# Optimization experiments

Measured on AMD Instinct MI355X. Metric: run time of the kernel, lower is better.

Reference implementation:

```python
import jax, jax.numpy as jnp
import numpy as np

B, S, D = 2, 1024, 2048
L = 4
HQ, HKV, HD = 32, 8, 64
I = 5632
V = 32000
EPS = 1e-5
THETA = 10000.0
SCALE = HD ** -0.5
GROUP = HQ // HKV


def setup_inputs() -> dict:
    key = jax.random.key(0)
    ks = jax.random.split(key, 8)
    s = 0.02
    return {
        "input_ids": jax.random.randint(ks[0], (B, S), 0, V, dtype=jnp.int32),
        "positions": jnp.broadcast_to(jnp.arange(S, dtype=jnp.int32), (B, S)),
        "embed": jax.random.normal(ks[1], (V, D), jnp.float32) * s,
        "w_qkv": jax.random.normal(ks[2], (L, D, (HQ + 2 * HKV) * HD), jnp.float32) * s,
        "w_o": jax.random.normal(ks[3], (L, HQ * HD, D), jnp.float32) * s,
        "w_gate_up": jax.random.normal(ks[4], (L, D, 2 * I), jnp.float32) * s,
        "w_down": jax.random.normal(ks[5], (L, I, D), jnp.float32) * s,
        "ln1_w": jnp.ones((L, D), jnp.float32),
        "ln2_w": jnp.ones((L, D), jnp.float32),
        "norm_w": jnp.ones((D,), jnp.float32),
    }


def rmsnorm(x, w):
    var = jnp.mean(x * x, axis=-1, keepdims=True)
    return x * jax.lax.rsqrt(var + EPS) * w


def rope(positions, x):
    # x: [B, S, H, HD]; neox-style rotate-half RoPE
    inv_freq = 1.0 / (THETA ** (jnp.arange(0, HD, 2, dtype=jnp.float32) / HD))
    ang = positions.astype(jnp.float32)[..., None] * inv_freq  # [B, S, HD/2]
    cos = jnp.cos(ang)[:, :, None, :]
    sin = jnp.sin(ang)[:, :, None, :]
    x1, x2 = jnp.split(x, 2, axis=-1)
    return jnp.concatenate([x1 * cos - x2 * sin, x2 * cos + x1 * sin], axis=-1)


def llama_forward(input_ids, positions, embed, w_qkv, w_o, w_gate_up, w_down,
                  ln1_w, ln2_w, norm_w):
    h = embed[input_ids]                      # [B, S, D]
    res = jnp.zeros_like(h)
    causal = jnp.tril(jnp.ones((S, S), dtype=bool))
    neg = jnp.asarray(jnp.finfo(h.dtype).min, h.dtype)

    def layer(carry, params):
        h, res = carry
        wqkv, wo, wgu, wd, l1, l2 = params
        # fused RMSNorm + residual-add (vllm RMSNorm(x, residual) semantics)
        res = h + res
        h = rmsnorm(res, l1)
        # QKV projection + RoPE
        qkv = h @ wqkv
        q, k, v = jnp.split(qkv, [HQ * HD, (HQ + HKV) * HD], axis=-1)
        q = q.reshape(B, S, HQ, HD)
        k = k.reshape(B, S, HKV, HD)
        v = v.reshape(B, S, HKV, HD)
        q = rope(positions, q)
        k = rope(positions, k)
        # GQA: broadcast kv heads across query groups
        k = jnp.repeat(k, GROUP, axis=2)      # [B, S, HQ, HD]
        v = jnp.repeat(v, GROUP, axis=2)
        scores = jnp.einsum('bqhd,bkhd->bhqk', q, k) * SCALE
        scores = jnp.where(causal, scores, neg)
        attn = jax.nn.softmax(scores, axis=-1)
        o = jnp.einsum('bhqk,bkhd->bqhd', attn, v).reshape(B, S, HQ * HD)
        h = o @ wo
        # post-attention fused RMSNorm + residual
        res = h + res
        h = rmsnorm(res, l2)
        # SwiGLU MLP
        gu = h @ wgu
        g, u = jnp.split(gu, 2, axis=-1)
        h = (jax.nn.silu(g) * u) @ wd
        return (h, res), None

    (h, res), _ = jax.lax.scan(layer, (h, res),
                               (w_qkv, w_o, w_gate_up, w_down, ln1_w, ln2_w))
    return rmsnorm(h + res, norm_w)


def reference(input_ids, positions, embed, w_qkv, w_o, w_gate_up, w_down,
              ln1_w, ln2_w, norm_w):
    return llama_forward(input_ids, positions, embed, w_qkv, w_o, w_gate_up,
                         w_down, ln1_w, ln2_w, norm_w)
```

## Files before the change

### kernel.cpp

```cpp
#include <hip/hip_runtime.h>
#include <hip/hip_bf16.h>

#define B_ 2
#define S_ 1024
#define T_ (B_*S_)
#define D_ 2048
#define L_ 4
#define HQ_ 32
#define HKV_ 8
#define HD_ 64
#define I_ 5632
#define EPS_ 1e-5f
#define SCALE_ 0.125f

typedef __attribute__((ext_vector_type(4))) float  float4v;
typedef __attribute__((ext_vector_type(8))) short  short8v;

#define GLOAD16(g, l) \
  __builtin_amdgcn_global_load_lds((const __attribute__((address_space(1))) void*)(g), \
                                   (__attribute__((address_space(3))) void*)(l), 16, 0, 0)

__device__ __forceinline__ short f2bf(float f) {
  union { float f; unsigned u; } c; c.f = f;
  unsigned u = c.u + 0x7fffu + ((c.u >> 16) & 1u);
  return (short)(u >> 16);
}

__device__ __forceinline__ void xcd_swizzle(int gx, int gy, int& bx, int& by) {
  int nwg = gx * gy;
  int orig = by * gx + bx;
  int q = nwg >> 3, r = nwg & 7;
  int xcd = orig & 7, loc = orig >> 3;
  int swz = (xcd < r ? xcd * (q + 1) : r * (q + 1) + (xcd - r) * q) + loc;
  bx = swz / gy;
  by = swz - bx * gy;
}

__global__ __launch_bounds__(256)
void transpose_bf16(const float* __restrict__ in, short* __restrict__ out,
                    int K, int N) {
  __shared__ float t[64][65];
  const int bx = blockIdx.x * 64;
  const int by = blockIdx.y * 64;
  const int tid = threadIdx.x;
  const int lr = tid >> 4;
  const int lc = (tid & 15) * 4;
  #pragma unroll
  for (int j = 0; j < 64; j += 16) {
    float4v v = *(const float4v*)(in + (size_t)(by + lr + j) * N + bx + lc);
    t[lr + j][lc] = v[0]; t[lr + j][lc + 1] = v[1];
    t[lr + j][lc + 2] = v[2]; t[lr + j][lc + 3] = v[3];
  }
  __syncthreads();
  const int nr = tid >> 3;
  const int kc = (tid & 7) * 8;
  #pragma unroll
  for (int j = 0; j < 64; j += 32) {
    short8v y;
    #pragma unroll
    for (int e = 0; e < 8; e++) y[e] = f2bf(t[kc + e][nr + j]);
    *(short8v*)(out + (size_t)(bx + nr + j) * K + by + kc) = y;
  }
}

__global__ __launch_bounds__(256)
void embed_gather(const int* __restrict__ ids, const float* __restrict__ embed,
                  float* __restrict__ h) {
  size_t i = (size_t)blockIdx.x * 256 + threadIdx.x;
  int t  = (int)(i >> 9);
  int d4 = (int)(i & 511);
  ((float4v*)h)[i] = ((const float4v*)(embed + (size_t)ids[t] * D_))[d4];
}

__global__ __launch_bounds__(256)
void rmsnorm_kernel(const float* __restrict__ x, float* __restrict__ res,
                    const float* __restrict__ w, void* __restrict__ outp,
                    int first, int bf16out) {
  const int row = blockIdx.x;
  const int tid = threadIdx.x;
  const size_t base = (size_t)row * D_;
  float4v v0, v1;
  if (first) {
    v0 = ((const float4v*)(x + base))[tid * 2];
    v1 = ((const float4v*)(x + base))[tid * 2 + 1];
    ((float4v*)(res + base))[tid * 2]     = v0;
    ((float4v*)(res + base))[tid * 2 + 1] = v1;
  } else {
    v0 = ((const float4v*)(res + base))[tid * 2];
    v1 = ((const float4v*)(res + base))[tid * 2 + 1];
  }
  float ss = v0[0]*v0[0] + v0[1]*v0[1] + v0[2]*v0[2] + v0[3]*v0[3]
           + v1[0]*v1[0] + v1[1]*v1[1] + v1[2]*v1[2] + v1[3]*v1[3];
  #pragma unroll
  for (int off = 32; off > 0; off >>= 1) ss += __shfl_xor(ss, off, 64);
  __shared__ float red[4];
  if ((tid & 63) == 0) red[tid >> 6] = ss;
  __syncthreads();
  float tot = red[0] + red[1] + red[2] + red[3];
  float rs = rsqrtf(tot * (1.0f / D_) + EPS_);
  float4v w0 = ((const float4v*)w)[tid * 2];
  float4v w1 = ((const float4v*)w)[tid * 2 + 1];
  float4v o0 = v0 * rs * w0;
  float4v o1 = v1 * rs * w1;
  if (bf16out) {
    short8v y;
    #pragma unroll
    for (int k = 0; k < 4; k++) { y[k] = f2bf(o0[k]); y[k + 4] = f2bf(o1[k]); }
    ((short8v*)((char*)outp + base * 2))[tid] = y;
  } else {
    float* op = (float*)outp + base;
    ((float4v*)op)[tid * 2]     = o0;
    ((float4v*)op)[tid * 2 + 1] = o1;
  }
}

__global__ __launch_bounds__(512, 4)
void gemm_big128(const short* __restrict__ A, const short* __restrict__ Bt,
                 float* __restrict__ C, int M, int N, int K, int addto) {
  __shared__ short sA[2][128 * 64];
  __shared__ short sB[2][128 * 64];
  int bx = blockIdx.x, by = blockIdx.y;
  xcd_swizzle(gridDim.x, gridDim.y, bx, by);
  const int tid  = threadIdx.x;
  const int lane = tid & 63;
  const int wv   = tid >> 6;
  const int wr   = wv >> 2;
  const int wc   = wv & 3;
  const int row0 = by * 128;
  const int col0 = bx * 128;
  const int fr = lane & 15;
  const int g  = lane >> 4;
  const int NT = K >> 6;

  float4v acc[4][2] = {};

  int rS[2], cS[2];
  #pragma unroll
  for (int k = 0; k < 2; k++) {
    int s = tid + k * 512;
    rS[k] = s >> 3;
    cS[k] = (((s & 7) ^ (rS[k] & 7)) << 3);
  }

#define STAGE128(t, buf) do { \
    int k0_ = (t) << 6; \
    _Pragma("unroll") \
    for (int k_ = 0; k_ < 2; k_++) \
      GLOAD16(A  + (size_t)(row0 + rS[k_]) * K + k0_ + cS[k_], \
              &sA[buf][(tid + k_ * 512) * 8]); \
    _Pragma("unroll") \
    for (int k_ = 0; k_ < 2; k_++) \
      GLOAD16(Bt + (size_t)(col0 + rS[k_]) * K + k0_ + cS[k_], \
              &sB[buf][(tid + k_ * 512) * 8]); \
  } while (0)

  STAGE128(0, 0);

  for (int t = 0; t < NT; t++) {
    const int cur = t & 1;
    if (t + 1 < NT) {
      STAGE128(t + 1, cur ^ 1);
      asm volatile("s_waitcnt vmcnt(4)" ::: "memory");
    } else {
      asm volatile("s_waitcnt vmcnt(0)" ::: "memory");
    }
    __builtin_amdgcn_s_barrier();
    __builtin_amdgcn_sched_barrier(0);

    const short* pA = &sA[cur][(wr * 64) * 64];
    const short* pB = &sB[cur][(wc * 32) * 64];
    #pragma unroll
    for (int ks = 0; ks < 2; ks++) {
      const int fswk = ((((ks << 2) | g) ^ (fr & 7)) << 3);
      short8v bfr[2], afr[4];
      #pragma unroll
      for (int ni = 0; ni < 2; ni++)
        bfr[ni] = *(const short8v*)(pB + (ni * 16 + fr) * 64 + fswk);
      #pragma unroll
      for (int m4 = 0; m4 < 4; m4++)
        afr[m4] = *(const short8v*)(pA + (m4 * 16 + fr) * 64 + fswk);
      __builtin_amdgcn_s_setprio(1);
      #pragma unroll
      for (int m4 = 0; m4 < 4; m4++)
        #pragma unroll
        for (int ni = 0; ni < 2; ni++)
          acc[m4][ni] = __builtin_amdgcn_mfma_f32_16x16x32_bf16(
              afr[m4], bfr[ni], acc[m4][ni], 0, 0, 0);
      __builtin_amdgcn_s_setprio(0);
    }
    asm volatile("" ::: "memory");
    __builtin_amdgcn_s_barrier();
  }

  #pragma unroll
  for (int m4 = 0; m4 < 4; m4++)
    #pragma unroll
    for (int ni = 0; ni < 2; ni++) {
      size_t base = (size_t)(row0 + wr * 64 + m4 * 16 + g * 4) * N
                    + col0 + wc * 32 + ni * 16 + fr;
      if (addto) {
        #pragma unroll
        for (int r = 0; r < 4; r++)
          C[base + (size_t)r * N] += acc[m4][ni][r];
      } else {
        #pragma unroll
        for (int r = 0; r < 4; r++)
          C[base + (size_t)r * N] = acc[m4][ni][r];
      }
    }
#undef STAGE128
}

__global__ __launch_bounds__(512, 2)
void gemm_glu_big(const short* __restrict__ A, const short* __restrict__ Bt,
                  short* __restrict__ mlp, int K) {
  __shared__ short sA[2][128 * 64];
  __shared__ short sG[2][128 * 64];
  __shared__ short sU[2][128 * 64];
  int bx = blockIdx.x, by = blockIdx.y;
  xcd_swizzle(gridDim.x, gridDim.y, bx, by);
  const int tid  = threadIdx.x;
  const int lane = tid & 63;
  const int wv   = tid >> 6;
  const int wr   = wv >> 2;
  const int wc   = wv & 3;
  const int row0 = by * 128;
  const int col0 = bx * 128;
  const int fr = lane & 15;
  const int g  = lane >> 4;
  const int NT = K >> 6;

  float4v accg[4][2] = {};
  float4v accu[4][2] = {};

  int rS[2], cS[2];
  #pragma unroll
  for (int k = 0; k < 2; k++) {
    int s = tid + k * 512;
    rS[k] = s >> 3;
    cS[k] = (((s & 7) ^ (rS[k] & 7)) << 3);
  }

#define STAGEGLU(t, buf) do { \
    int k0_ = (t) << 6; \
    _Pragma("unroll") \
    for (int k_ = 0; k_ < 2; k_++) \
      GLOAD16(A  + (size_t)(row0 + rS[k_]) * K + k0_ + cS[k_], \
              &sA[buf][(tid + k_ * 512) * 8]); \
    _Pragma("unroll") \
    for (int k_ = 0; k_ < 2; k_++) \
      GLOAD16(Bt + (size_t)(col0 + rS[k_]) * K + k0_ + cS[k_], \
              &sG[buf][(tid + k_ * 512) * 8]); \
    _Pragma("unroll") \
    for (int k_ = 0; k_ < 2; k_++) \
      GLOAD16(Bt + (size_t)(col0 + I_ + rS[k_]) * K + k0_ + cS[k_], \
              &sU[buf][(tid + k_ * 512) * 8]); \
  } while (0)

  STAGEGLU(0, 0);

  for (int t = 0; t < NT; t++) {
    const int cur = t & 1;
    if (t + 1 < NT) {
      STAGEGLU(t + 1, cur ^ 1);
      asm volatile("s_waitcnt vmcnt(6)" ::: "memory");
    } else {
      asm volatile("s_waitcnt vmcnt(0)" ::: "memory");
    }
    __builtin_amdgcn_s_barrier();
    __builtin_amdgcn_sched_barrier(0);

    const short* pA = &sA[cur][(wr * 64) * 64];
    const short* pG = &sG[cur][(wc * 32) * 64];
    const short* pU = &sU[cur][(wc * 32) * 64];
    #pragma unroll
    for (int ks = 0; ks < 2; ks++) {
      const int fswk = ((((ks << 2) | g) ^ (fr & 7)) << 3);
      short8v bg[2], bu[2], afr[4];
      #pragma unroll
      for (int ni = 0; ni < 2; ni++) {
        bg[ni] = *(const short8v*)(pG + (ni * 16 + fr) * 64 + fswk);
        bu[ni] = *(const short8v*)(pU + (ni * 16 + fr) * 64 + fswk);
      }
      #pragma unroll
      for (int m4 = 0; m4 < 4; m4++)
        afr[m4] = *(const short8v*)(pA + (m4 * 16 + fr) * 64 + fswk);
      __builtin_amdgcn_s_setprio(1);
      #pragma unroll
      for (int m4 = 0; m4 < 4; m4++)
        #pragma unroll
        for (int ni = 0; ni < 2; ni++) {
          accg[m4][ni] = __builtin_amdgcn_mfma_f32_16x16x32_bf16(
              afr[m4], bg[ni], accg[m4][ni], 0, 0, 0);
          accu[m4][ni] = __builtin_amdgcn_mfma_f32_16x16x32_bf16(
              afr[m4], bu[ni], accu[m4][ni], 0, 0, 0);
        }
      __builtin_amdgcn_s_setprio(0);
    }
    asm volatile("" ::: "memory");
    __builtin_amdgcn_s_barrier();
  }

  #pragma unroll
  for (int m4 = 0; m4 < 4; m4++)
    #pragma unroll
    for (int ni = 0; ni < 2; ni++) {
      size_t base = (size_t)(row0 + wr * 64 + m4 * 16 + g * 4) * I_
                    + col0 + wc * 32 + ni * 16 + fr;
      #pragma unroll
      for (int r = 0; r < 4; r++) {
        float gv = accg[m4][ni][r], uv = accu[m4][ni][r];
        mlp[base + (size_t)r * I_] = f2bf(gv / (1.0f + __expf(-gv)) * uv);
      }
    }
#undef STAGEGLU
}

__global__ __launch_bounds__(512, 4)
void gemm_qkv_big(const short* __restrict__ A, const short* __restrict__ Bt,
                  const float* __restrict__ tab, short* __restrict__ qbf,
                  short* __restrict__ kbf, short* __restrict__ vbf, int K) {
  __shared__ short sA[2][128 * 64];
  __shared__ short sB[2][128 * 64];
  int bx = blockIdx.x, by = blockIdx.y;
  xcd_swizzle(gridDim.x, gridDim.y, bx, by);
  const int tid  = threadIdx.x;
  const int lane = tid & 63;
  const int wv   = tid >> 6;
  const int wm   = (wv >> 1) * 32;
  const int wn   = (wv & 1) * 64;
  const int row0 = by * 128;
  const int col0 = bx * 128;
  const int fr = lane & 15;
  const int g  = lane >> 4;
  const int NT = K >> 6;

  float4v acc[2][4] = {};

  int rS[2], cS[2];
  #pragma unroll
  for (int k = 0; k < 2; k++) {
    int s = tid + k * 512;
    rS[k] = s >> 3;
    cS[k] = (((s & 7) ^ (rS[k] & 7)) << 3);
  }

#define STAGEQKV(t, buf) do { \
    int k0_ = (t) << 6; \
    _Pragma("unroll") \
    for (int k_ = 0; k_ < 2; k_++) \
      GLOAD16(A  + (size_t)(row0 + rS[k_]) * K + k0_ + cS[k_], \
              &sA[buf][(tid + k_ * 512) * 8]); \
    _Pragma("unroll") \
    for (int k_ = 0; k_ < 2; k_++) \
      GLOAD16(Bt + (size_t)(col0 + rS[k_]) * K + k0_ + cS[k_], \
              &sB[buf][(tid + k_ * 512) * 8]); \
  } while (0)

  STAGEQKV(0, 0);

  for (int t = 0; t < NT; t++) {
    const int cur = t & 1;
    if (t + 1 < NT) {
      STAGEQKV(t + 1, cur ^ 1);
      asm volatile("s_waitcnt vmcnt(4)" ::: "memory");
    } else {
      asm volatile("s_waitcnt vmcnt(0)" ::: "memory");
    }
    __builtin_amdgcn_s_barrier();
    __builtin_amdgcn_sched_barrier(0);

    const short* pA = &sA[cur][wm * 64];
    const short* pB = &sB[cur][wn * 64];
    #pragma unroll
    for (int ks = 0; ks < 2; ks++) {
      const int fswk = ((((ks << 2) | g) ^ (fr & 7)) << 3);
      short8v afr[2], bfr[4];
      #pragma unroll
      for (int m2 = 0; m2 < 2; m2++)
        afr[m2] = *(const short8v*)(pA + (m2 * 16 + fr) * 64 + fswk);
      #pragma unroll
      for (int ni = 0; ni < 4; ni++)
        bfr[ni] = *(const short8v*)(pB + (ni * 16 + fr) * 64 + fswk);
      __builtin_amdgcn_s_setprio(1);
      #pragma unroll
      for (int m2 = 0; m2 < 2; m2++)
        #pragma unroll
        for (int ni = 0; ni < 4; ni++)
          acc[m2][ni] = __builtin_amdgcn_mfma_f32_16x16x32_bf16(
              afr[m2], bfr[ni], acc[m2][ni], 0, 0, 0);
      __builtin_amdgcn_s_setprio(0);
    }
    asm volatile("" ::: "memory");
    __builtin_amdgcn_s_barrier();
  }

  const int head = (col0 + wn) >> 6;
  if (head < HQ_ + HKV_) {
    const float sc = (head < HQ_) ? SCALE_ : 1.0f;
    short* dst = (head < HQ_) ? qbf : kbf;
    const int hh = (head < HQ_) ? head : head - HQ_;
    const int HN = (head < HQ_) ? HQ_ : HKV_;
    #pragma unroll
    for (int m2 = 0; m2 < 2; m2++)
      #pragma unroll
      for (int jj = 0; jj < 2; jj++)
        #pragma unroll
        for (int r = 0; r < 4; r++) {
          int m = row0 + wm + m2 * 16 + g * 4 + r;
          int b = m >> 10, s = m & (S_ - 1);
          int d1 = jj * 16 + fr;
          float x1 = acc[m2][jj][r], x2 = acc[m2][jj + 2][r];
          const float* tb = tab + (size_t)m * 64 + d1 * 2;
          float c = tb[0], sn = tb[1];
          size_t base = ((size_t)((b * HN + hh) * S_ + s)) * HD_;
          dst[base + d1]      = f2bf((x1 * c - x2 * sn) * sc);
          dst[base + d1 + 32] = f2bf((x2 * c + x1 * sn) * sc);
        }
  } else {
    const int vh = head - HQ_ - HKV_;
    #pragma unroll
    for (int m2 = 0; m2 < 2; m2++)
      #pragma unroll
      for (int ni = 0; ni < 4; ni++)
        #pragma unroll
        for (int r = 0; r < 4; r++) {
          int m = row0 + wm + m2 * 16 + g * 4 + r;
          int b = m >> 10, s = m & (S_ - 1);
          vbf[((size_t)((b * HKV_ + vh) * S_ + s)) * HD_ + ni * 16 + fr] =
              f2bf(acc[m2][ni][r]);
        }
  }
#undef STAGEQKV
}

__global__ __launch_bounds__(256)
void rope_table(const int* __restrict__ pos, float* __restrict__ tab) {
  int i = blockIdx.x * 256 + threadIdx.x;
  int t = i >> 5, ii = i & 31;
  float p = (float)pos[t];
  float freq = __expf(-(float)ii * (9.210340371976184f / 32.0f));
  float ang = p * freq;
  tab[2 * i]     = cosf(ang);
  tab[2 * i + 1] = sinf(ang);
}

#define KPAD 68

__global__ __launch_bounds__(256)
void transpose_v(const short* __restrict__ vbf, short* __restrict__ vtbf) {
  __shared__ short sv[64 * KPAD];
  const int jt = blockIdx.x, kh = blockIdx.y, b = blockIdx.z;
  const int tid = threadIdx.x;
  const short* src = vbf + ((size_t)((b * HKV_ + kh) * S_ + jt * 64)) * HD_;
  #pragma unroll
  for (int it = 0; it < 2; it++) {
    int c = it * 256 + tid;
    int rr = c >> 3, ch = (c & 7) * 8;
    *(short8v*)(&sv[rr * KPAD + ch]) = *(const short8v*)(src + (size_t)rr * HD_ + ch);
  }
  __syncthreads();
  const int dc = tid >> 2;
  const int jc = (tid & 3) * 16;
  short8v o1, o2;
  #pragma unroll
  for (int k = 0; k < 8; k++) o1[k] = sv[(jc + k) * KPAD + dc];
  #pragma unroll
  for (int k = 0; k < 8; k++) o2[k] = sv[(jc + 8 + k) * KPAD + dc];
  short* od = vtbf + ((size_t)((b * HKV_ + kh) * HD_ + dc)) * S_ + jt * 64 + jc;
  *(short8v*)od       = o1;
  *(short8v*)(od + 8) = o2;
}

__global__ __launch_bounds__(256)
void attn_mfma(const short* __restrict__ qbf, const short* __restrict__ kbf,
               const short* __restrict__ vtbf, short* __restrict__ obf) {
  __shared__ short sK[64 * KPAD];
  __shared__ short sVt[64 * KPAD];
  __shared__ short sP[4][16 * KPAD];
  const int qb = blockIdx.x;
  const int h  = blockIdx.y;
  const int b  = blockIdx.z;
  const int kh = h >> 2;
  const int tid  = threadIdx.x;
  const int lane = tid & 63;
  const int wv   = tid >> 6;
  const int q0 = qb * 64;
  const int cc = lane & 15;
  const int g  = lane >> 4;

  short8v qf0, qf1;
  {
    const short* qrow = qbf + ((size_t)((b * HQ_ + h) * S_ + q0 + wv * 16 + cc)) * HD_;
    qf0 = *(const short8v*)(qrow + g * 8);
    qf1 = *(const short8v*)(qrow + g * 8 + 32);
  }
  float4v accO[4] = {};
  float m_r[4], l_r[4];
  #pragma unroll
  for (int r = 0; r < 4; r++) { m_r[r] = -1e30f; l_r[r] = 0.f; }

  const short* kb = kbf  + ((size_t)(b * HKV_ + kh)) * S_ * HD_;
  const short* vb = vtbf + ((size_t)(b * HKV_ + kh)) * HD_ * S_;

  const int rr0 = tid >> 3;
  const int ch0 = (tid & 7) * 8;
  const int rr1 = 32 + rr0;

  short8v kr0 = *(const short8v*)(kb + (size_t)rr0 * HD_ + ch0);
  short8v kr1 = *(const short8v*)(kb + (size_t)rr1 * HD_ + ch0);
  short8v vr0 = *(const short8v*)(vb + (size_t)rr0 * S_ + ch0);
  short8v vr1 = *(const short8v*)(vb + (size_t)rr1 * S_ + ch0);

  for (int jt = 0; jt <= qb; jt++) {
    const int j0 = jt * 64;
    __syncthreads();
    *(short8v*)(&sK[rr0 * KPAD + ch0])  = kr0;
    *(short8v*)(&sK[rr1 * KPAD + ch0])  = kr1;
    *(short8v*)(&sVt[rr0 * KPAD + ch0]) = vr0;
    *(short8v*)(&sVt[rr1 * KPAD + ch0]) = vr1;
    __syncthreads();

    if (jt < qb) {
      const int j0n = j0 + 64;
      kr0 = *(const short8v*)(kb + (size_t)(j0n + rr0) * HD_ + ch0);
      kr1 = *(const short8v*)(kb + (size_t)(j0n + rr1) * HD_ + ch0);
      vr0 = *(const short8v*)(vb + (size_t)rr0 * S_ + j0n + ch0);
      vr1 = *(const short8v*)(vb + (size_t)rr1 * S_ + j0n + ch0);
    }

    float4v sc[4] = {};
    #pragma unroll
    for (int ct = 0; ct < 4; ct++) {
      short8v k0 = *(const short8v*)(&sK[(ct * 16 + cc) * KPAD + g * 8]);
      short8v k1 = *(const short8v*)(&sK[(ct * 16 + cc) * KPAD + g * 8 + 32]);
      __builtin_amdgcn_s_setprio(1);
      sc[ct] = __builtin_amdgcn_mfma_f32_16x16x32_bf16(qf0, k0, sc[ct], 0, 0, 0);
      sc[ct] = __builtin_amdgcn_mfma_f32_16x16x32_bf16(qf1, k1, sc[ct], 0, 0, 0);
      __builtin_amdgcn_s_setprio(0);
    }
    if (jt == qb) {
      #pragma unroll
      for (int ct = 0; ct < 4; ct++)
        #pragma unroll
        for (int r = 0; r < 4; r++)
          if (j0 + ct * 16 + cc > q0 + wv * 16 + g * 4 + r) sc[ct][r] = -1e30f;
    }
    float pmv[4], dmax = -1e30f;
    #pragma unroll
    for (int r = 0; r < 4; r++) {
      float pm = fmaxf(fmaxf(sc[0][r], sc[1][r]), fmaxf(sc[2][r], sc[3][r]));
      pm = fmaxf(pm, __shfl_xor(pm, 1, 64));
      pm = fmaxf(pm, __shfl_xor(pm, 2, 64));
      pm = fmaxf(pm, __shfl_xor(pm, 4, 64));
      pm = fmaxf(pm, __shfl_xor(pm, 8, 64));
      pmv[r] = pm;
      dmax = fmaxf(dmax, pm - m_r[r]);
    }
    if (!__all(dmax <= 8.0f)) {
      float corr[4];
      #pragma unroll
      for (int r = 0; r < 4; r++) {
        float mn = fmaxf(m_r[r], pmv[r]);
        corr[r] = __expf(m_r[r] - mn);
        m_r[r] = mn;
        l_r[r] *= corr[r];
      }
      #pragma unroll
      for (int dt = 0; dt < 4; dt++)
        #pragma unroll
        for (int r = 0; r < 4; r++)
          accO[dt][r] *= corr[r];
    }
    #pragma unroll
    for (int r = 0; r < 4; r++) {
      float rs = 0.f;
      #pragma unroll
      for (int ct = 0; ct < 4; ct++) {
        float p = __expf(sc[ct][r] - m_r[r]);
        sc[ct][r] = p;
        rs += p;
      }
      rs += __shfl_xor(rs, 1, 64);
      rs += __shfl_xor(rs, 2, 64);
      rs += __shfl_xor(rs, 4, 64);
      rs += __shfl_xor(rs, 8, 64);
      l_r[r] += rs;
    }
    #pragma unroll
    for (int ct = 0; ct < 4; ct++)
      #pragma unroll
      for (int r = 0; r < 4; r++)
        sP[wv][(g * 4 + r) * KPAD + ct * 16 + cc] = f2bf(sc[ct][r]);
    short8v pf0 = *(const short8v*)(&sP[wv][cc * KPAD + g * 8]);
    short8v pf1 = *(const short8v*)(&sP[wv][cc * KPAD + g * 8 + 32]);
    #pragma unroll
    for (int dt = 0; dt < 4; dt++) {
      short8v v0 = *(const short8v*)(&sVt[(dt * 16 + cc) * KPAD + g * 8]);
      short8v v1 = *(const short8v*)(&sVt[(dt * 16 + cc) * KPAD + g * 8 + 32]);
      __builtin_amdgcn_s_setprio(1);
      accO[dt] = __builtin_amdgcn_mfma_f32_16x16x32_bf16(pf0, v0, accO[dt], 0, 0, 0);
      accO[dt] = __builtin_amdgcn_mfma_f32_16x16x32_bf16(pf1, v1, accO[dt], 0, 0, 0);
      __builtin_amdgcn_s_setprio(0);
    }
  }
  #pragma unroll
  for (int dt = 0; dt < 4; dt++)
    #pragma unroll
    for (int r = 0; r < 4; r++) {
      int q = q0 + wv * 16 + g * 4 + r;
      obf[((size_t)(b * S_ + q)) * 2048 + h * 64 + dt * 16 + cc] = f2bf(accO[dt][r] / l_r[r]);
    }
}

extern "C" void kernel_launch(void* const* d_in, const int* in_sizes, int n_in,
                              void* d_out, int out_size, void* d_ws, size_t ws_size,
                              hipStream_t stream) {
  const int*   ids   = (const int*)d_in[0];
  const int*   pos   = (const int*)d_in[1];
  const float* embed = (const float*)d_in[2];
  const float* w_qkv = (const float*)d_in[3];
  const float* w_o   = (const float*)d_in[4];
  const float* w_gu  = (const float*)d_in[5];
  const float* w_dn  = (const float*)d_in[6];
  const float* ln1   = (const float*)d_in[7];
  const float* ln2   = (const float*)d_in[8];
  const float* normw = (const float*)d_in[9];
  float* out = (float*)d_out;

  char* p = (char*)d_ws;
  short* wT    = (short*)p; p += (size_t)11264 * 2048 * 2;
  float* h     = (float*)p; p += (size_t)T_ * D_ * 4;
  float* res   = (float*)p; p += (size_t)T_ * D_ * 4;
  short* hnbf  = (short*)p; p += (size_t)T_ * D_ * 2;
  short* obf   = (short*)p; p += (size_t)T_ * D_ * 2;
  short* mlpbf = (short*)p; p += (size_t)T_ * I_ * 2;
  float* tab   = (float*)p; p += (size_t)T_ * 64 * 4;
  short* qbf   = (short*)p; p += (size_t)B_ * HQ_ * S_ * HD_ * 2;
  short* kbf   = (short*)p; p += (size_t)B_ * HKV_ * S_ * HD_ * 2;
  short* vbf   = (short*)p; p += (size_t)B_ * HKV_ * S_ * HD_ * 2;
  short* vtbf  = (short*)p; p += (size_t)B_ * HKV_ * HD_ * S_ * 2;

  embed_gather<<<T_ * D_ / 4 / 256, 256, 0, stream>>>(ids, embed, h);
  rope_table<<<T_ * 32 / 256, 256, 0, stream>>>(pos, tab);

  for (int l = 0; l < L_; l++) {
    rmsnorm_kernel<<<T_, 256, 0, stream>>>(h, res, ln1 + l * D_, hnbf,
                                           l == 0 ? 1 : 0, 1);

    transpose_bf16<<<dim3(3072 / 64, 2048 / 64), 256, 0, stream>>>(
        w_qkv + (size_t)l * 2048 * 3072, wT, 2048, 3072);
    gemm_qkv_big<<<dim3(3072 / 128, T_ / 128), 512, 0, stream>>>(
        hnbf, wT, tab, qbf, kbf, vbf, 2048);

    transpose_v<<<dim3(16, 8, 2), 256, 0, stream>>>(vbf, vtbf);
    attn_mfma<<<dim3(16, 32, 2), 256, 0, stream>>>(qbf, kbf, vtbf, obf);

    transpose_bf16<<<dim3(2048 / 64, 2048 / 64), 256, 0, stream>>>(
        w_o + (size_t)l * 2048 * 2048, wT, 2048, 2048);
    gemm_big128<<<dim3(2048 / 128, T_ / 128), 512, 0, stream>>>(
        obf, wT, res, T_, 2048, 2048, 1);

    rmsnorm_kernel<<<T_, 256, 0, stream>>>(nullptr, res, ln2 + l * D_, hnbf, 0, 1);

    transpose_bf16<<<dim3(11264 / 64, 2048 / 64), 256, 0, stream>>>(
        w_gu + (size_t)l * 2048 * 11264, wT, 2048, 11264);
    gemm_glu_big<<<dim3(I_ / 128, T_ / 128), 512, 0, stream>>>(
        hnbf, wT, mlpbf, 2048);

    transpose_bf16<<<dim3(2048 / 64, 5632 / 64), 256, 0, stream>>>(
        w_dn + (size_t)l * 5632 * 2048, wT, 5632, 2048);
    gemm_big128<<<dim3(2048 / 128, T_ / 128), 512, 0, stream>>>(
        mlpbf, wT, res, T_, 2048, 5632, 1);
  }
  rmsnorm_kernel<<<T_, 256, 0, stream>>>(nullptr, res, normw, out, 0, 0);
}
```

Baseline: 1.739 ms.

## Batch weight transposes into one launch, fuse V transpose, widen attention blocks

Transposes and converts to bf16 the weights of all four layers in a single kernel launch, writing them into dedicated per-layer workspace buffers instead of running sixteen separate transposes inside the layer loop. The QKV GEMM epilogue now writes V directly in transposed layout, so the separate transpose_v kernel is removed. Attention blocks grow to 512 threads covering 128 queries each, which halves the block count and shares each K/V tile load across more waves. The cost is a larger workspace and a new causal-mask condition over the last two key tiles of each block.

```diff
diff --git a/kernel.cpp b/kernel.cpp
--- a/kernel.cpp
+++ b/kernel.cpp
@@ -15,6 +15,7 @@
 
 typedef __attribute__((ext_vector_type(4))) float  float4v;
 typedef __attribute__((ext_vector_type(8))) short  short8v;
+typedef __attribute__((ext_vector_type(4))) short  short4v;
 
 #define GLOAD16(g, l) \
   __builtin_amdgcn_global_load_lds((const __attribute__((address_space(1))) void*)(g), \
@@ -37,11 +38,24 @@
 }
 
 __global__ __launch_bounds__(256)
-void transpose_bf16(const float* __restrict__ in, short* __restrict__ out,
-                    int K, int N) {
+void transpose_all(const float* __restrict__ wq, const float* __restrict__ wo,
+                   const float* __restrict__ wg, const float* __restrict__ wd,
+                   short* __restrict__ tq, short* __restrict__ to_,
+                   short* __restrict__ tg, short* __restrict__ td) {
+  const int l = blockIdx.y;
+  int id = blockIdx.x;
+  const float* in; short* out; int K, N, bxt, byt;
+  if (id < 1536)      { in = wq + (size_t)l * 2048 * 3072;  out = tq + (size_t)l * 2048 * 3072;
+                        K = 2048; N = 3072;  bxt = id % 48;  byt = id / 48; }
+  else if (id < 2560) { id -= 1536; in = wo + (size_t)l * 2048 * 2048; out = to_ + (size_t)l * 2048 * 2048;
+                        K = 2048; N = 2048;  bxt = id % 32;  byt = id / 32; }
+  else if (id < 8192) { id -= 2560; in = wg + (size_t)l * 2048 * 11264; out = tg + (size_t)l * 2048 * 11264;
+                        K = 2048; N = 11264; bxt = id % 176; byt = id / 176; }
+  else                { id -= 8192; in = wd + (size_t)l * 5632 * 2048; out = td + (size_t)l * 5632 * 2048;
+                        K = 5632; N = 2048;  bxt = id % 32;  byt = id / 32; }
   __shared__ float t[64][65];
-  const int bx = blockIdx.x * 64;
-  const int by = blockIdx.y * 64;
+  const int bx = bxt * 64;
+  const int by = byt * 64;
   const int tid = threadIdx.x;
   const int lr = tid >> 4;
   const int lc = (tid & 15) * 4;
@@ -319,7 +333,7 @@
 __global__ __launch_bounds__(512, 4)
 void gemm_qkv_big(const short* __restrict__ A, const short* __restrict__ Bt,
                   const float* __restrict__ tab, short* __restrict__ qbf,
-                  short* __restrict__ kbf, short* __restrict__ vbf, int K) {
+                  short* __restrict__ kbf, short* __restrict__ vtbf, int K) {
   __shared__ short sA[2][128 * 64];
   __shared__ short sB[2][128 * 64];
   int bx = blockIdx.x, by = blockIdx.y;
@@ -420,16 +434,18 @@
   } else {
     const int vh = head - HQ_ - HKV_;
     #pragma unroll
-    for (int m2 = 0; m2 < 2; m2++)
-      #pragma unroll
-      for (int ni = 0; ni < 4; ni++)
-        #pragma unroll
-        for (int r = 0; r < 4; r++) {
-          int m = row0 + wm + m2 * 16 + g * 4 + r;
-          int b = m >> 10, s = m & (S_ - 1);
-          vbf[((size_t)((b * HKV_ + vh) * S_ + s)) * HD_ + ni * 16 + fr] =
-              f2bf(acc[m2][ni][r]);
-        }
+    for (int m2 = 0; m2 < 2; m2++) {
+      int m0 = row0 + wm + m2 * 16 + g * 4;
+      int b = m0 >> 10, s0 = m0 & (S_ - 1);
+      #pragma unroll
+      for (int ni = 0; ni < 4; ni++) {
+        int d = ni * 16 + fr;
+        short4v w;
+        #pragma unroll
+        for (int r = 0; r < 4; r++) w[r] = f2bf(acc[m2][ni][r]);
+        *(short4v*)(&vtbf[((size_t)((b * HKV_ + vh) * HD_ + d)) * S_ + s0]) = w;
+      }
+    }
   }
 #undef STAGEQKV
 }
@@ -447,37 +463,12 @@
 
 #define KPAD 68
 
-__global__ __launch_bounds__(256)
-void transpose_v(const short* __restrict__ vbf, short* __restrict__ vtbf) {
-  __shared__ short sv[64 * KPAD];
-  const int jt = blockIdx.x, kh = blockIdx.y, b = blockIdx.z;
-  const int tid = threadIdx.x;
-  const short* src = vbf + ((size_t)((b * HKV_ + kh) * S_ + jt * 64)) * HD_;
-  #pragma unroll
-  for (int it = 0; it < 2; it++) {
-    int c = it * 256 + tid;
-    int rr = c >> 3, ch = (c & 7) * 8;
-    *(short8v*)(&sv[rr * KPAD + ch]) = *(const short8v*)(src + (size_t)rr * HD_ + ch);
-  }
-  __syncthreads();
-  const int dc = tid >> 2;
-  const int jc = (tid & 3) * 16;
-  short8v o1, o2;
-  #pragma unroll
-  for (int k = 0; k < 8; k++) o1[k] = sv[(jc + k) * KPAD + dc];
-  #pragma unroll
-  for (int k = 0; k < 8; k++) o2[k] = sv[(jc + 8 + k) * KPAD + dc];
-  short* od = vtbf + ((size_t)((b * HKV_ + kh) * HD_ + dc)) * S_ + jt * 64 + jc;
-  *(short8v*)od       = o1;
-  *(short8v*)(od + 8) = o2;
-}
-
-__global__ __launch_bounds__(256)
+__global__ __launch_bounds__(512)
 void attn_mfma(const short* __restrict__ qbf, const short* __restrict__ kbf,
                const short* __restrict__ vtbf, short* __restrict__ obf) {
   __shared__ short sK[64 * KPAD];
   __shared__ short sVt[64 * KPAD];
-  __shared__ short sP[4][16 * KPAD];
+  __shared__ short sP[8][16 * KPAD];
   const int qb = blockIdx.x;
   const int h  = blockIdx.y;
   const int b  = blockIdx.z;
@@ -485,7 +476,7 @@
   const int tid  = threadIdx.x;
   const int lane = tid & 63;
   const int wv   = tid >> 6;
-  const int q0 = qb * 64;
+  const int q0 = qb * 128;
   const int cc = lane & 15;
   const int g  = lane >> 4;
 
@@ -503,30 +494,24 @@
   const short* kb = kbf  + ((size_t)(b * HKV_ + kh)) * S_ * HD_;
   const short* vb = vtbf + ((size_t)(b * HKV_ + kh)) * HD_ * S_;
 
-  const int rr0 = tid >> 3;
-  const int ch0 = (tid & 7) * 8;
-  const int rr1 = 32 + rr0;
-
-  short8v kr0 = *(const short8v*)(kb + (size_t)rr0 * HD_ + ch0);
-  short8v kr1 = *(const short8v*)(kb + (size_t)rr1 * HD_ + ch0);
-  short8v vr0 = *(const short8v*)(vb + (size_t)rr0 * S_ + ch0);
-  short8v vr1 = *(const short8v*)(vb + (size_t)rr1 * S_ + ch0);
-
-  for (int jt = 0; jt <= qb; jt++) {
+  const int rr = tid >> 3;
+  const int ch = (tid & 7) * 8;
+
+  short8v kr = *(const short8v*)(kb + (size_t)rr * HD_ + ch);
+  short8v vr = *(const short8v*)(vb + (size_t)rr * S_ + ch);
+
+  const int nb = 2 * qb + 1;
+  for (int jt = 0; jt <= nb; jt++) {
     const int j0 = jt * 64;
     __syncthreads();
-    *(short8v*)(&sK[rr0 * KPAD + ch0])  = kr0;
-    *(short8v*)(&sK[rr1 * KPAD + ch0])  = kr1;
-    *(short8v*)(&sVt[rr0 * KPAD + ch0]) = vr0;
-    *(short8v*)(&sVt[rr1 * KPAD + ch0]) = vr1;
+    *(short8v*)(&sK[rr * KPAD + ch])  = kr;
+    *(short8v*)(&sVt[rr * KPAD + ch]) = vr;
     __syncthreads();
 
-    if (jt < qb) {
+    if (jt < nb) {
       const int j0n = j0 + 64;
-      kr0 = *(const short8v*)(kb + (size_t)(j0n + rr0) * HD_ + ch0);
-      kr1 = *(const short8v*)(kb + (size_t)(j0n + rr1) * HD_ + ch0);
-      vr0 = *(const short8v*)(vb + (size_t)rr0 * S_ + j0n + ch0);
-      vr1 = *(const short8v*)(vb + (size_t)rr1 * S_ + j0n + ch0);
+      kr = *(const short8v*)(kb + (size_t)(j0n + rr) * HD_ + ch);
+      vr = *(const short8v*)(vb + (size_t)rr * S_ + j0n + ch);
     }
 
     float4v sc[4] = {};
@@ -539,7 +524,7 @@
       sc[ct] = __builtin_amdgcn_mfma_f32_16x16x32_bf16(qf1, k1, sc[ct], 0, 0, 0);
       __builtin_amdgcn_s_setprio(0);
     }
-    if (jt == qb) {
+    if (jt >= 2 * qb) {
       #pragma unroll
       for (int ct = 0; ct < 4; ct++)
         #pragma unroll
@@ -629,7 +614,10 @@
   float* out = (float*)d_out;
 
   char* p = (char*)d_ws;
-  short* wT    = (short*)p; p += (size_t)11264 * 2048 * 2;
+  short* wTq  = (short*)p; p += (size_t)L_ * 2048 * 3072 * 2;
+  short* wTo  = (short*)p; p += (size_t)L_ * 2048 * 2048 * 2;
+  short* wTgu = (short*)p; p += (size_t)L_ * 2048 * 11264 * 2;
+  short* wTdn = (short*)p; p += (size_t)L_ * 5632 * 2048 * 2;
   float* h     = (float*)p; p += (size_t)T_ * D_ * 4;
   float* res   = (float*)p; p += (size_t)T_ * D_ * 4;
   short* hnbf  = (short*)p; p += (size_t)T_ * D_ * 2;
@@ -638,9 +626,10 @@
   float* tab   = (float*)p; p += (size_t)T_ * 64 * 4;
   short* qbf   = (short*)p; p += (size_t)B_ * HQ_ * S_ * HD_ * 2;
   short* kbf   = (short*)p; p += (size_t)B_ * HKV_ * S_ * HD_ * 2;
-  short* vbf   = (short*)p; p += (size_t)B_ * HKV_ * S_ * HD_ * 2;
   short* vtbf  = (short*)p; p += (size_t)B_ * HKV_ * HD_ * S_ * 2;
 
+  transpose_all<<<dim3(11008, L_), 256, 0, stream>>>(
+      w_qkv, w_o, w_gu, w_dn, wTq, wTo, wTgu, wTdn);
   embed_gather<<<T_ * D_ / 4 / 256, 256, 0, stream>>>(ids, embed, h);
   rope_table<<<T_ * 32 / 256, 256, 0, stream>>>(pos, tab);
 
@@ -648,30 +637,21 @@
     rmsnorm_kernel<<<T_, 256, 0, stream>>>(h, res, ln1 + l * D_, hnbf,
                                            l == 0 ? 1 : 0, 1);
 
-    transpose_bf16<<<dim3(3072 / 64, 2048 / 64), 256, 0, stream>>>(
-        w_qkv + (size_t)l * 2048 * 3072, wT, 2048, 3072);
     gemm_qkv_big<<<dim3(3072 / 128, T_ / 128), 512, 0, stream>>>(
-        hnbf, wT, tab, qbf, kbf, vbf, 2048);
-
-    transpose_v<<<dim3(16, 8, 2), 256, 0, stream>>>(vbf, vtbf);
-    attn_mfma<<<dim3(16, 32, 2), 256, 0, stream>>>(qbf, kbf, vtbf, obf);
-
-    transpose_bf16<<<dim3(2048 / 64, 2048 / 64), 256, 0, stream>>>(
-        w_o + (size_t)l * 2048 * 2048, wT, 2048, 2048);
+        hnbf, wTq + (size_t)l * 2048 * 3072, tab, qbf, kbf, vtbf, 2048);
+
+    attn_mfma<<<dim3(8, 32, 2), 512, 0, stream>>>(qbf, kbf, vtbf, obf);
+
     gemm_big128<<<dim3(2048 / 128, T_ / 128), 512, 0, stream>>>(
-        obf, wT, res, T_, 2048, 2048, 1);
+        obf, wTo + (size_t)l * 2048 * 2048, res, T_, 2048, 2048, 1);
 
     rmsnorm_kernel<<<T_, 256, 0, stream>>>(nullptr, res, ln2 + l * D_, hnbf, 0, 1);
 
-    transpose_bf16<<<dim3(11264 / 64, 2048 / 64), 256, 0, stream>>>(
-        w_gu + (size_t)l * 2048 * 11264, wT, 2048, 11264);
     gemm_glu_big<<<dim3(I_ / 128, T_ / 128), 512, 0, stream>>>(
-        hnbf, wT, mlpbf, 2048);
-
-    transpose_bf16<<<dim3(2048 / 64, 5632 / 64), 256, 0, stream>>>(
-        w_dn + (size_t)l * 5632 * 2048, wT, 5632, 2048);
+        hnbf, wTgu + (size_t)l * 2048 * 11264, mlpbf, 2048);
+
     gemm_big128<<<dim3(2048 / 128, T_ / 128), 512, 0, stream>>>(
-        mlpbf, wT, res, T_, 2048, 5632, 1);
+        mlpbf, wTdn + (size_t)l * 5632 * 2048, res, T_, 2048, 5632, 1);
   }
   rmsnorm_kernel<<<T_, 256, 0, stream>>>(nullptr, res, normw, out, 0, 0);
 }
```

New measurement: 1.927 ms. 1.11x slower.
